# Kernel optimization log

Hardware: AMD Instinct MI355X
Metric: run time of the kernel (lower is better)

Reference implementation:

```python
import jax, jax.numpy as jnp
import numpy as np
import math


def _bandwidth(d):
    # gz = 2*Gamma((d+1)/2)/Gamma(d/2); use lgamma for numerical stability.
    gz = 2.0 * math.exp(math.lgamma(0.5 * (d + 1)) - math.lgamma(0.5 * d))
    return 1.0 / (2.0 * gz * gz)


def _kernel_mean(xa, xb, gamma):
    # mean over the [Na, Nb] RBF kernel matrix, squared distance via matmul identity
    sq = (jnp.sum(xa * xa, axis=1)[:, None]
          + jnp.sum(xb * xb, axis=1)[None, :]
          - 2.0 * (xa @ xb.T))
    sq = jnp.maximum(sq, 0.0)  # guard tiny negatives from the identity
    return jnp.mean(jnp.exp(-gamma * sq))


def setup_inputs() -> dict:
    key = jax.random.key(0)
    k1, k2 = jax.random.split(key)
    x1 = jax.random.normal(k1, (8192, 128), dtype=jnp.float32)
    x2 = jax.random.normal(k2, (8192, 128), dtype=jnp.float32)
    return {"x1": x1, "x2": x2}


def reference(x1, x2):
    g1 = _bandwidth(x1.shape[1])
    g2 = _bandwidth(x2.shape[1])
    m11 = _kernel_mean(x1, x1, g1)
    m22 = _kernel_mean(x2, x2, g2)
    m12 = _kernel_mean(x1, x2, g1)
    return jnp.sqrt(m11 - 2.0 * m12 + m22)
```

## Files before the change

### kernel.cpp

```cpp
#include <hip/hip_runtime.h>
#include <cmath>

#define D 128
#define BM 128
#define BK 64
#define LOG2E 1.4426950408889634

typedef __attribute__((ext_vector_type(8))) _Float16 f16x8;
typedef __attribute__((ext_vector_type(4))) float f32x4;
typedef __attribute__((ext_vector_type(2))) float f32x2;

__device__ __forceinline__ void async_cp16(const void* g, void* l) {
    __builtin_amdgcn_global_load_lds(
        (__attribute__((address_space(1))) void*)g,
        (__attribute__((address_space(3))) void*)l, 16, 0, 0);
}

__global__ __launch_bounds__(256) void prep_kernel(
    const float* __restrict__ x1, const float* __restrict__ x2,
    _Float16* __restrict__ xh, float* __restrict__ El,
    double* __restrict__ acc, float gl, int N) {
    int tid = threadIdx.x;
    if (blockIdx.x == 0 && tid < 64) acc[tid] = 0.0;
    int r = blockIdx.x * 16 + (tid >> 4);
    if (r >= 2 * N) return;
    int l = tid & 15;
    const float* row = (r < N) ? x1 + (size_t)r * D : x2 + (size_t)(r - N) * D;
    float4 v0 = ((const float4*)row)[l * 2];
    float4 v1 = ((const float4*)row)[l * 2 + 1];
    float v[8] = {v0.x, v0.y, v0.z, v0.w, v1.x, v1.y, v1.z, v1.w};
    float p = 0.f;
    _Float16 h8[8];
#pragma unroll
    for (int j = 0; j < 8; ++j) {
        p = fmaf(v[j], v[j], p);
        h8[j] = (_Float16)v[j];
    }
    *(uint4*)(xh + (size_t)r * D + l * 8) = *(uint4*)h8;
#pragma unroll
    for (int off = 8; off; off >>= 1) p += __shfl_down(p, off, 16);
    if (l == 0) El[r] = gl * p;
}

__global__ __launch_bounds__(256, 4) void mmd_mfma_kernel(
    const _Float16* __restrict__ xh, const float* __restrict__ El,
    double* __restrict__ acc, float c2l, int N) {
    __shared__ float4 smem[2048];

    int t = blockIdx.x;
    int bi = (int)((sqrtf(8.0f * t + 1.0f) - 1.0f) * 0.5f);
    while ((bi + 1) * (bi + 2) / 2 <= t) ++bi;
    while (bi * (bi + 1) / 2 > t) --bi;
    int bj = t - bi * (bi + 1) / 2;

    int half = N / BM;
    float w = (bi == bj) ? 1.0f : 2.0f;
    if ((bi < half) != (bj < half)) w = -2.0f;
    int aBase = bi * BM, bBase = bj * BM;

    int tid = threadIdx.x;
    int lane = tid & 63, wave = tid >> 6;
    int quad = lane >> 4, l16 = lane & 15;
    int wrow = (wave & 1) * 64, wcol = (wave >> 1) * 64;

    const _Float16* gsrc[8];
    float4* ldst[8];
#pragma unroll
    for (int r = 0; r < 2; ++r) {
        int rowBase = r ? bBase : aBase;
#pragma unroll
        for (int i = 0; i < 4; ++i) {
            int slot = i * 256 + tid;
            int row = slot >> 3;
            int kc4 = (slot & 7) ^ (row & 7);
            gsrc[r * 4 + i] = xh + ((size_t)(rowBase + row) * D + kc4 * 8);
            ldst[r * 4 + i] = &smem[r * 1024 + slot];
        }
    }

    f32x4 C[4][4];
#pragma unroll
    for (int i = 0; i < 4; ++i)
#pragma unroll
        for (int j = 0; j < 4; ++j) C[i][j] = {0.f, 0.f, 0.f, 0.f};

    for (int c = 0; c < 2; ++c) {
        if (c) __syncthreads();
        int koff = c * BK;
#pragma unroll
        for (int q = 0; q < 8; ++q) async_cp16(gsrc[q] + koff, ldst[q]);
        __syncthreads();
#pragma unroll
        for (int s = 0; s < 2; ++s) {
            int kc4 = s * 4 + quad;
            f16x8 a[4], b[4];
#pragma unroll
            for (int u = 0; u < 4; ++u) {
                int ar = wrow + u * 16 + l16;
                a[u] = *(const f16x8*)&smem[ar * 8 + (kc4 ^ (ar & 7))];
                int br = wcol + u * 16 + l16;
                b[u] = *(const f16x8*)&smem[1024 + br * 8 + (kc4 ^ (br & 7))];
            }
#pragma unroll
            for (int ti = 0; ti < 4; ++ti)
#pragma unroll
                for (int tj = 0; tj < 4; ++tj)
                    C[ti][tj] = __builtin_amdgcn_mfma_f32_16x16x32_f16(
                        a[ti], b[tj], C[ti][tj], 0, 0, 0);
        }
    }

    int arow0 = aBase + wrow + quad * 4;
    int bcol0 = bBase + wcol + l16;
    float4 ea4[4];
#pragma unroll
    for (int ti = 0; ti < 4; ++ti) ea4[ti] = *(const float4*)&El[arow0 + ti * 16];
    f32x2 cc = {c2l, c2l};
    float lsum = 0.f;
#pragma unroll
    for (int tj = 0; tj < 4; ++tj) {
        float eb = El[bcol0 + tj * 16];
        f32x2 p = {0.f, 0.f};
#pragma unroll
        for (int ti = 0; ti < 4; ++ti) {
            f32x4 d = C[ti][tj];
            f32x2 a01 = cc * f32x2{d.x, d.y} + f32x2{ea4[ti].x, ea4[ti].y};
            f32x2 a23 = cc * f32x2{d.z, d.w} + f32x2{ea4[ti].z, ea4[ti].w};
            f32x2 e, e2;
            e.x = __builtin_amdgcn_exp2f(a01.x);
            e.y = __builtin_amdgcn_exp2f(a01.y);
            e2.x = __builtin_amdgcn_exp2f(a23.x);
            e2.y = __builtin_amdgcn_exp2f(a23.y);
            p += e + e2;
        }
        lsum = fmaf(p.x + p.y, __builtin_amdgcn_exp2f(eb), lsum);
    }
    double ds = (double)lsum * (double)w;
#pragma unroll
    for (int off = 32; off; off >>= 1) ds += __shfl_down(ds, off);
    __syncthreads();
    double* red = (double*)smem;
    if (lane == 0) red[wave] = ds;
    __syncthreads();
    if (tid == 0)
        atomicAdd(&acc[(bi + bj) & 63], red[0] + red[1] + red[2] + red[3]);
}

__global__ __launch_bounds__(64) void mmd_finalize_kernel(
    const double* __restrict__ acc, float* __restrict__ out, int N) {
    int l = threadIdx.x;
    double v = acc[l];
#pragma unroll
    for (int off = 32; off; off >>= 1) v += __shfl_down(v, off);
    if (l == 0) {
        double nn = (double)N * (double)N;
        double s = v / nn;
        out[0] = (float)sqrt(s > 0.0 ? s : 0.0);
    }
}

extern "C" void kernel_launch(void* const* d_in, const int* in_sizes, int n_in,
                              void* d_out, int out_size, void* d_ws, size_t ws_size,
                              hipStream_t stream) {
    const float* x1 = (const float*)d_in[0];
    const float* x2 = (const float*)d_in[1];
    int N = in_sizes[0] / D;

    double* acc = (double*)d_ws;
    float* El = (float*)((char*)d_ws + 8192);
    _Float16* xh = (_Float16*)((char*)d_ws + 73728);

    double lg = lgamma(0.5 * (D + 1)) - lgamma(0.5 * D);
    double gz = 2.0 * exp(lg);
    double gamma = 1.0 / (2.0 * gz * gz);
    float gl = (float)(-gamma * LOG2E);
    float c2l = (float)(2.0 * gamma * LOG2E);

    prep_kernel<<<(2 * N + 15) / 16, 256, 0, stream>>>(x1, x2, xh, El, acc, gl, N);

    int nt2 = 2 * N / BM;
    int nblocks = nt2 * (nt2 + 1) / 2;
    mmd_mfma_kernel<<<nblocks, 256, 0, stream>>>(xh, El, acc, c2l, N);

    mmd_finalize_kernel<<<1, 64, 0, stream>>>(acc, (float*)d_out, N);
}
```

Before: 108.8 us.

## Make MMD kernel persistent over paired triangle rows with double-buffered B tiles

```diff
diff --git a/kernel.cpp b/kernel.cpp
--- a/kernel.cpp
+++ b/kernel.cpp
@@ -3,7 +3,7 @@
 
 #define D 128
 #define BM 128
-#define BK 64
+#define NSEG 8
 #define LOG2E 1.4426950408889634
 
 typedef __attribute__((ext_vector_type(8))) _Float16 f16x8;
@@ -42,108 +42,149 @@
     if (l == 0) El[r] = gl * p;
 }
 
-__global__ __launch_bounds__(256, 4) void mmd_mfma_kernel(
+__global__ __launch_bounds__(256, 2) void mmd_mfma_kernel(
     const _Float16* __restrict__ xh, const float* __restrict__ El,
     double* __restrict__ acc, float c2l, int N) {
-    __shared__ float4 smem[2048];
-
-    int t = blockIdx.x;
-    int bi = (int)((sqrtf(8.0f * t + 1.0f) - 1.0f) * 0.5f);
-    while ((bi + 1) * (bi + 2) / 2 <= t) ++bi;
-    while (bi * (bi + 1) / 2 > t) --bi;
-    int bj = t - bi * (bi + 1) / 2;
-
-    int half = N / BM;
-    float w = (bi == bj) ? 1.0f : 2.0f;
-    if ((bi < half) != (bj < half)) w = -2.0f;
-    int aBase = bi * BM, bBase = bj * BM;
+    __shared__ float4 smem[2][2048];
 
     int tid = threadIdx.x;
     int lane = tid & 63, wave = tid >> 6;
     int quad = lane >> 4, l16 = lane & 15;
     int wrow = (wave & 1) * 64, wcol = (wave >> 1) * 64;
 
-    const _Float16* gsrc[8];
-    float4* ldst[8];
-#pragma unroll
-    for (int r = 0; r < 2; ++r) {
-        int rowBase = r ? bBase : aBase;
-#pragma unroll
-        for (int i = 0; i < 4; ++i) {
-            int slot = i * 256 + tid;
-            int row = slot >> 3;
-            int kc4 = (slot & 7) ^ (row & 7);
-            gsrc[r * 4 + i] = xh + ((size_t)(rowBase + row) * D + kc4 * 8);
-            ldst[r * 4 + i] = &smem[r * 1024 + slot];
-        }
-    }
-
-    f32x4 C[4][4];
-#pragma unroll
-    for (int i = 0; i < 4; ++i)
-#pragma unroll
-        for (int j = 0; j < 4; ++j) C[i][j] = {0.f, 0.f, 0.f, 0.f};
-
-    for (int c = 0; c < 2; ++c) {
-        if (c) __syncthreads();
-        int koff = c * BK;
-#pragma unroll
-        for (int q = 0; q < 8; ++q) async_cp16(gsrc[q] + koff, ldst[q]);
-        __syncthreads();
-#pragma unroll
-        for (int s = 0; s < 2; ++s) {
-            int kc4 = s * 4 + quad;
-            f16x8 a[4], b[4];
+    int nt2 = 2 * N / BM;
+    int half = N / BM;
+    int p = blockIdx.x >> 3;
+    int s = blockIdx.x & (NSEG - 1);
+    int tpp = nt2 + 1;
+    int q = tpp / NSEG, r = tpp % NSEG;
+    int t0 = s * q + (s < r ? s : r);
+    int nt = q + (s < r ? 1 : 0);
+
+    int goff[8], lslot[8];
+#pragma unroll
+    for (int i = 0; i < 8; ++i) {
+        int slot = i * 256 + tid;
+        int row = slot >> 4;
+        int g = (slot & 15) ^ (row & 7);
+        goff[i] = row * D + g * 8;
+        lslot[i] = slot;
+    }
+
+    auto stage = [&](int bBase, int buf) {
+        const _Float16* src = xh + (size_t)bBase * D;
+#pragma unroll
+        for (int i = 0; i < 8; ++i)
+            async_cp16(src + goff[i], &smem[buf][lslot[i]]);
+    };
+    auto BI = [&](int tt) { return tt <= p ? p : nt2 - 1 - p; };
+    auto BJ = [&](int tt) { return tt <= p ? tt : tt - p - 1; };
+
+    stage(BJ(t0) * BM, 0);
+    stage(BJ(t0 + 1) * BM, 1);
+
+    f16x8 a[4][4];
+    float4 ea4[4];
+    int curA = -1;
+    double dsum = 0.0;
+
+    for (int i = 0; i < nt; ++i) {
+        int tt = t0 + i;
+        int bi = BI(tt), bj = BJ(tt);
+        int aBase = bi * BM, bBase = bj * BM;
+        float w = (bi == bj) ? 1.0f : 2.0f;
+        if ((bi < half) != (bj < half)) w = -2.0f;
+        int cur = i & 1;
+
+        if (i + 1 < nt) {
+            asm volatile("s_waitcnt vmcnt(8)" ::: "memory");
+        } else {
+            asm volatile("s_waitcnt vmcnt(0)" ::: "memory");
+        }
+        __builtin_amdgcn_s_barrier();
+        __builtin_amdgcn_sched_barrier(0);
+
+        if (aBase != curA) {
+            curA = aBase;
 #pragma unroll
             for (int u = 0; u < 4; ++u) {
-                int ar = wrow + u * 16 + l16;
-                a[u] = *(const f16x8*)&smem[ar * 8 + (kc4 ^ (ar & 7))];
+                int ar = aBase + wrow + u * 16 + l16;
+#pragma unroll
+                for (int j = 0; j < 4; ++j) {
+                    int g = (j >> 1) * 8 + (j & 1) * 4 + quad;
+                    a[u][j] = *(const f16x8*)(xh + (size_t)ar * D + g * 8);
+                }
+            }
+            int arow0 = aBase + wrow + quad * 4;
+#pragma unroll
+            for (int ti = 0; ti < 4; ++ti)
+                ea4[ti] = *(const float4*)&El[arow0 + ti * 16];
+        }
+
+        int bcol0 = bBase + wcol + l16;
+        float ebv[4];
+#pragma unroll
+        for (int tj = 0; tj < 4; ++tj) ebv[tj] = El[bcol0 + tj * 16];
+
+        f32x4 C[4][4];
+#pragma unroll
+        for (int ti = 0; ti < 4; ++ti)
+#pragma unroll
+            for (int tj = 0; tj < 4; ++tj) C[ti][tj] = {0.f, 0.f, 0.f, 0.f};
+
+#pragma unroll
+        for (int j = 0; j < 4; ++j) {
+            int gb = (j >> 1) * 8 + (j & 1) * 4 + quad;
+            f16x8 b[4];
+#pragma unroll
+            for (int u = 0; u < 4; ++u) {
                 int br = wcol + u * 16 + l16;
-                b[u] = *(const f16x8*)&smem[1024 + br * 8 + (kc4 ^ (br & 7))];
+                b[u] = *(const f16x8*)&smem[cur][br * 16 + (gb ^ (br & 7))];
             }
+            __builtin_amdgcn_s_setprio(1);
 #pragma unroll
             for (int ti = 0; ti < 4; ++ti)
 #pragma unroll
                 for (int tj = 0; tj < 4; ++tj)
                     C[ti][tj] = __builtin_amdgcn_mfma_f32_16x16x32_f16(
-                        a[ti], b[tj], C[ti][tj], 0, 0, 0);
-        }
-    }
-
-    int arow0 = aBase + wrow + quad * 4;
-    int bcol0 = bBase + wcol + l16;
-    float4 ea4[4];
-#pragma unroll
-    for (int ti = 0; ti < 4; ++ti) ea4[ti] = *(const float4*)&El[arow0 + ti * 16];
-    f32x2 cc = {c2l, c2l};
-    float lsum = 0.f;
-#pragma unroll
-    for (int tj = 0; tj < 4; ++tj) {
-        float eb = El[bcol0 + tj * 16];
-        f32x2 p = {0.f, 0.f};
-#pragma unroll
-        for (int ti = 0; ti < 4; ++ti) {
-            f32x4 d = C[ti][tj];
-            f32x2 a01 = cc * f32x2{d.x, d.y} + f32x2{ea4[ti].x, ea4[ti].y};
-            f32x2 a23 = cc * f32x2{d.z, d.w} + f32x2{ea4[ti].z, ea4[ti].w};
-            f32x2 e, e2;
-            e.x = __builtin_amdgcn_exp2f(a01.x);
-            e.y = __builtin_amdgcn_exp2f(a01.y);
-            e2.x = __builtin_amdgcn_exp2f(a23.x);
-            e2.y = __builtin_amdgcn_exp2f(a23.y);
-            p += e + e2;
-        }
-        lsum = fmaf(p.x + p.y, __builtin_amdgcn_exp2f(eb), lsum);
-    }
-    double ds = (double)lsum * (double)w;
-#pragma unroll
-    for (int off = 32; off; off >>= 1) ds += __shfl_down(ds, off);
-    __syncthreads();
-    double* red = (double*)smem;
-    if (lane == 0) red[wave] = ds;
+                        a[ti][j], b[tj], C[ti][tj], 0, 0, 0);
+            __builtin_amdgcn_s_setprio(0);
+        }
+
+        f32x2 cc = {c2l, c2l};
+        float lsum = 0.f;
+#pragma unroll
+        for (int tj = 0; tj < 4; ++tj) {
+            f32x2 p2 = {0.f, 0.f};
+#pragma unroll
+            for (int ti = 0; ti < 4; ++ti) {
+                f32x4 d = C[ti][tj];
+                f32x2 a01 = cc * f32x2{d.x, d.y} + f32x2{ea4[ti].x, ea4[ti].y};
+                f32x2 a23 = cc * f32x2{d.z, d.w} + f32x2{ea4[ti].z, ea4[ti].w};
+                f32x2 e, e2;
+                e.x = __builtin_amdgcn_exp2f(a01.x);
+                e.y = __builtin_amdgcn_exp2f(a01.y);
+                e2.x = __builtin_amdgcn_exp2f(a23.x);
+                e2.y = __builtin_amdgcn_exp2f(a23.y);
+                p2 += e + e2;
+            }
+            lsum = fmaf(p2.x + p2.y, __builtin_amdgcn_exp2f(ebv[tj]), lsum);
+        }
+        dsum += (double)lsum * (double)w;
+
+        __builtin_amdgcn_sched_barrier(0);
+        __builtin_amdgcn_s_barrier();
+        __builtin_amdgcn_sched_barrier(0);
+        if (i + 2 < nt) stage(BJ(tt + 2) * BM, cur);
+    }
+
+#pragma unroll
+    for (int off = 32; off; off >>= 1) dsum += __shfl_down(dsum, off);
+    double* red = (double*)&smem[0][0];
+    if (lane == 0) red[wave] = dsum;
     __syncthreads();
     if (tid == 0)
-        atomicAdd(&acc[(bi + bj) & 63], red[0] + red[1] + red[2] + red[3]);
+        atomicAdd(&acc[blockIdx.x & 63], red[0] + red[1] + red[2] + red[3]);
 }
 
 __global__ __launch_bounds__(64) void mmd_finalize_kernel(
@@ -179,7 +220,7 @@
     prep_kernel<<<(2 * N + 15) / 16, 256, 0, stream>>>(x1, x2, xh, El, acc, gl, N);
 
     int nt2 = 2 * N / BM;
-    int nblocks = nt2 * (nt2 + 1) / 2;
+    int nblocks = (nt2 / 2) * NSEG;
     mmd_mfma_kernel<<<nblocks, 256, 0, stream>>>(xh, El, acc, c2l, N);
 
     mmd_finalize_kernel<<<1, 64, 0, stream>>>(acc, (float*)d_out, N);
```

After: 106.8 us. About the same (-1.9%).
